# Kernel optimization log

Measured on AMD Instinct MI355X. Metric: run time of the kernel, lower is better.

## Reference

```python
import jax, jax.numpy as jnp
import numpy as np

B, S, V, D, E, F, H, HS, TOPK = 8, 512, 32000, 1024, 8, 4096, 8, 128, 2
NEG = -1e9


def _ln(x, g, b):
    m = x.mean(-1, keepdims=True)
    v = jnp.var(x, axis=-1, keepdims=True)
    return (x - m) * jax.lax.rsqrt(v + 1e-5) * g + b


def _attn(x, Wq, Wk, Wv, Wo, bo):
    q = (x @ Wq).reshape(B, S, H, HS)
    k = (x @ Wk).reshape(B, S, H, HS)
    v = (x @ Wv).reshape(B, S, H, HS)
    att = jnp.einsum('bqhd,bkhd->bhqk', q, k) * (HS ** -0.5)
    causal = jnp.tril(jnp.ones((S, S), bool))
    att = jax.nn.softmax(jnp.where(causal, att, NEG), axis=-1)
    o = jnp.einsum('bhqk,bkhd->bqhd', att, v).reshape(B, S, H * HS)
    return o @ Wo + bo


def _moe(x, noise, Wr, br, Wn, bn, W1, b1, W2, b2):
    # NoisyTopkRouter: logits + randn * softplus(noise_logits), top-k, -inf fill, softmax
    logits = x @ Wr + br                                   # [B,S,E]
    noisy = logits + noise * jax.nn.softplus(x @ Wn + bn)
    _, idx = jax.lax.top_k(noisy, TOPK)                    # [B,S,K]
    mask = jax.nn.one_hot(idx, E, dtype=jnp.bool_).any(-2)  # [B,S,E]
    gate = jax.nn.softmax(jnp.where(mask, noisy, NEG), axis=-1)
    # dense all-expert FFN; combine with gate (gate==0 for non-selected experts,
    # so this equals the original sparse per-expert dispatch/scatter math)
    xf = x.reshape(-1, D)                                   # [T,D]
    gf = gate.reshape(-1, E)                                # [T,E]
    h = jax.nn.relu(jnp.einsum('td,edf->etf', xf, W1) + b1[:, None, :])
    y = jnp.einsum('etf,efd->etd', h, W2) + b2[:, None, :]
    out = jnp.einsum('etd,te->td', y, gf).reshape(x.shape)
    return out, gate


def setup_inputs() -> dict:
    key = jax.random.key(0)
    ks = jax.random.split(key, 24)
    n = lambda i, shp, sc=0.02: jax.random.normal(ks[i], shp, jnp.float32) * sc
    return dict(
        input_ids=jax.random.randint(ks[0], (B, S), 0, V),
        attention_mask=jnp.ones((B, S), jnp.int32),
        emb=n(1, (V, D), 1.0),
        pos=n(2, (1, S, D), 1.0),
        Wq=n(3, (D, H * HS)), Wk=n(4, (D, H * HS)), Wv=n(5, (D, H * HS)),
        Wo=n(6, (H * HS, D)), bo=jnp.zeros((D,)),
        g1=jnp.ones((D,)), be1=jnp.zeros((D,)),
        g2=jnp.ones((D,)), be2=jnp.zeros((D,)),
        g3=jnp.ones((D,)), be3=jnp.zeros((D,)),
        Wr1=n(7, (D, E)), br1=jnp.zeros((E,)), Wn1=n(8, (D, E)), bn1=jnp.zeros((E,)),
        W1a=n(9, (E, D, F)), b1a=jnp.zeros((E, F)), W2a=n(10, (E, F, D)), b2a=jnp.zeros((E, D)),
        Wr2=n(11, (D, E)), br2=jnp.zeros((E,)), Wn2=n(12, (D, E)), bn2=jnp.zeros((E,)),
        W1b=n(13, (E, D, F)), b1b=jnp.zeros((E, F)), W2b=n(14, (E, F, D)), b2b=jnp.zeros((E, D)),
        noise1=jax.random.normal(ks[15], (B, S, E), jnp.float32),
        noise2=jax.random.normal(ks[16], (B, S, E), jnp.float32),
        Wc=n(17, (D, 10)), bc=jnp.zeros((10,)),
    )


def reference(input_ids, attention_mask, emb, pos, Wq, Wk, Wv, Wo, bo,
              g1, be1, g2, be2, g3, be3,
              Wr1, br1, Wn1, bn1, W1a, b1a, W2a, b2a,
              Wr2, br2, Wn2, bn2, W1b, b1b, W2b, b2b,
              noise1, noise2, Wc, bc):
    x = emb[input_ids]                                     # [B,S,D]
    x = x + _attn(_ln(x, g1, be1), Wq, Wk, Wv, Wo, bo)
    x = x + pos                                            # dropout = identity (eval)
    first, _ = _moe(_ln(x, g2, be2), noise1, Wr1, br1, Wn1, bn1, W1a, b1a, W2a, b2a)
    second, _ = _moe(_ln(x, g3, be3), noise2, Wr2, br2, Wn2, bn2, W1b, b1b, W2b, b2b)
    feature = second.mean(axis=1)                          # [B,D]
    cls = feature @ Wc + bc                                # [B,10]
    return (first, second, feature, cls)
```

## Files before the change

kernel.cpp:

```cpp
#include <hip/hip_runtime.h>
#include <cstdint>

typedef unsigned short u16;
typedef __attribute__((ext_vector_type(8))) __bf16 bf16x8;
typedef __attribute__((ext_vector_type(4))) float f32x4;

#define TOK 4096
#define DM  1024
#define EXP 8
#define FF  4096
#define SEQ 512
#define NH  8
#define HD  128
#define JOBCAP 18432

__device__ __forceinline__ u16 f2bf(float f) {
  union { float f; unsigned int u; } v; v.f = f;
  unsigned int u = v.u;
  u += 0x7FFFu + ((u >> 16) & 1u);
  return (u16)(u >> 16);
}
__device__ __forceinline__ float bf2f(u16 h) {
  union { unsigned int u; float f; } v; v.u = ((unsigned int)h) << 16; return v.f;
}

__device__ __forceinline__ void gl_lds16(const u16* g, u16* l) {
  __builtin_amdgcn_global_load_lds(
      (const __attribute__((address_space(1))) unsigned int*)g,
      (__attribute__((address_space(3))) unsigned int*)l, 16, 0, 0);
}

__global__ void k_embed(const int* __restrict__ ids, const float* __restrict__ emb,
                        float* __restrict__ x) {
  int t = blockIdx.x;
  int id = ids[t];
  const float4* src = (const float4*)(emb + (size_t)id * DM);
  float4* dst = (float4*)(x + (size_t)t * DM);
  dst[threadIdx.x] = src[threadIdx.x];
}

__global__ void k_lnrouter(const float* __restrict__ xin, const float* __restrict__ g,
                           const float* __restrict__ be,
                           const float* __restrict__ Wr, const float* __restrict__ br,
                           const float* __restrict__ Wn, const float* __restrict__ bn,
                           const float* __restrict__ noise,
                           u16* __restrict__ obf,
                           float* __restrict__ gates, int* __restrict__ topidx) {
  int t = blockIdx.x, tid = threadIdx.x;
  float4 v = ((const float4*)(xin + (size_t)t * DM))[tid];
  float s = v.x + v.y + v.z + v.w;
  float sq = v.x*v.x + v.y*v.y + v.z*v.z + v.w*v.w;
  for (int o = 32; o; o >>= 1) { s += __shfl_down(s, o); sq += __shfl_down(sq, o); }
  __shared__ float ss[4], sqs[4];
  if ((tid & 63) == 0) { ss[tid >> 6] = s; sqs[tid >> 6] = sq; }
  __syncthreads();
  s  = ss[0] + ss[1] + ss[2] + ss[3];
  sq = sqs[0] + sqs[1] + sqs[2] + sqs[3];
  float mean = s * (1.f / DM);
  float var  = sq * (1.f / DM) - mean * mean;
  float rstd = rsqrtf(var + 1e-5f);
  float4 gg = ((const float4*)g)[tid];
  float4 bb = ((const float4*)be)[tid];
  float xl[4];
  xl[0] = (v.x - mean) * rstd * gg.x + bb.x;
  xl[1] = (v.y - mean) * rstd * gg.y + bb.y;
  xl[2] = (v.z - mean) * rstd * gg.z + bb.z;
  xl[3] = (v.w - mean) * rstd * gg.w + bb.w;
  ushort4 u;
  u.x = f2bf(xl[0]); u.y = f2bf(xl[1]); u.z = f2bf(xl[2]); u.w = f2bf(xl[3]);
  ((ushort4*)(obf + (size_t)t * DM))[tid] = u;

  float pl[8], pn[8];
  #pragma unroll
  for (int e = 0; e < 8; e++) { pl[e] = 0.f; pn[e] = 0.f; }
  #pragma unroll
  for (int j = 0; j < 4; j++) {
    int d = tid * 4 + j;
    float xv = xl[j];
    const float4* wr = (const float4*)(Wr + (size_t)d * 8);
    const float4* wn = (const float4*)(Wn + (size_t)d * 8);
    float4 a0 = wr[0], a1 = wr[1], c0 = wn[0], c1 = wn[1];
    pl[0] += xv * a0.x; pl[1] += xv * a0.y; pl[2] += xv * a0.z; pl[3] += xv * a0.w;
    pl[4] += xv * a1.x; pl[5] += xv * a1.y; pl[6] += xv * a1.z; pl[7] += xv * a1.w;
    pn[0] += xv * c0.x; pn[1] += xv * c0.y; pn[2] += xv * c0.z; pn[3] += xv * c0.w;
    pn[4] += xv * c1.x; pn[5] += xv * c1.y; pn[6] += xv * c1.z; pn[7] += xv * c1.w;
  }
  for (int o = 32; o; o >>= 1) {
    #pragma unroll
    for (int e = 0; e < 8; e++) { pl[e] += __shfl_down(pl[e], o); pn[e] += __shfl_down(pn[e], o); }
  }
  __shared__ float sl[4][8], sn[4][8];
  if ((tid & 63) == 0) {
    int w = tid >> 6;
    #pragma unroll
    for (int e = 0; e < 8; e++) { sl[w][e] = pl[e]; sn[w][e] = pn[e]; }
  }
  __syncthreads();
  if (tid == 0) {
    float noisy[8];
    #pragma unroll
    for (int e = 0; e < 8; e++) {
      float l  = sl[0][e] + sl[1][e] + sl[2][e] + sl[3][e] + br[e];
      float nn = sn[0][e] + sn[1][e] + sn[2][e] + sn[3][e] + bn[e];
      float sp = (nn > 20.f) ? nn : log1pf(expf(nn));
      noisy[e] = l + noise[(size_t)t * 8 + e] * sp;
    }
    int i0 = 0;
    for (int e = 1; e < 8; e++) if (noisy[e] > noisy[i0]) i0 = e;
    int i1 = (i0 == 0) ? 1 : 0;
    for (int e = 0; e < 8; e++) if (e != i0 && noisy[e] > noisy[i1]) i1 = e;
    float e1 = expf(noisy[i1] - noisy[i0]);
    float zz = 1.f + e1;
    gates[t * 2] = 1.f / zz; gates[t * 2 + 1] = e1 / zz;
    topidx[t * 2] = i0; topidx[t * 2 + 1] = i1;
  }
}

__global__ void k_ln2(const float* __restrict__ in, const float* __restrict__ g,
                      const float* __restrict__ be, u16* __restrict__ oh,
                      u16* __restrict__ ol) {
  int t = blockIdx.x, tid = threadIdx.x;
  float4 v = ((const float4*)(in + (size_t)t * DM))[tid];
  float s = v.x + v.y + v.z + v.w;
  float sq = v.x*v.x + v.y*v.y + v.z*v.z + v.w*v.w;
  for (int o = 32; o; o >>= 1) { s += __shfl_down(s, o); sq += __shfl_down(sq, o); }
  __shared__ float ss[4], sqs[4];
  if ((tid & 63) == 0) { ss[tid >> 6] = s; sqs[tid >> 6] = sq; }
  __syncthreads();
  s  = ss[0] + ss[1] + ss[2] + ss[3];
  sq = sqs[0] + sqs[1] + sqs[2] + sqs[3];
  float mean = s * (1.f / DM);
  float var  = sq * (1.f / DM) - mean * mean;
  float rstd = rsqrtf(var + 1e-5f);
  float4 gg = ((const float4*)g)[tid];
  float4 bb = ((const float4*)be)[tid];
  float o4[4];
  o4[0] = (v.x - mean) * rstd * gg.x + bb.x;
  o4[1] = (v.y - mean) * rstd * gg.y + bb.y;
  o4[2] = (v.z - mean) * rstd * gg.z + bb.z;
  o4[3] = (v.w - mean) * rstd * gg.w + bb.w;
  ushort4 uh, ul;
  u16* ph = (u16*)&uh; u16* pl = (u16*)&ul;
  #pragma unroll
  for (int i = 0; i < 4; i++) {
    u16 hi = f2bf(o4[i]); ph[i] = hi; pl[i] = f2bf(o4[i] - bf2f(hi));
  }
  ((ushort4*)(oh + (size_t)t * DM))[tid] = uh;
  ((ushort4*)(ol + (size_t)t * DM))[tid] = ul;
}

__global__ void k_tcvt_split4(const float* __restrict__ Wq, const float* __restrict__ Wk,
                              const float* __restrict__ Wv, const float* __restrict__ Wo,
                              u16* __restrict__ qkvh, u16* __restrict__ qkvl,
                              u16* __restrict__ oh, u16* __restrict__ ol) {
  __shared__ float t[32][33];
  int z = blockIdx.z;
  const float* src = (z == 0) ? Wq : (z == 1) ? Wk : (z == 2) ? Wv : Wo;
  u16* dh = (z < 3) ? qkvh + (size_t)z * DM * DM : oh;
  u16* dl = (z < 3) ? qkvl + (size_t)z * DM * DM : ol;
  int k0 = blockIdx.x * 32, n0 = blockIdx.y * 32;
  int tx = threadIdx.x, ty = threadIdx.y;
  #pragma unroll
  for (int i = 0; i < 4; i++) t[ty + 8*i][tx] = src[(size_t)(k0 + ty + 8*i) * DM + n0 + tx];
  __syncthreads();
  int u = ty * 32 + tx;
  int r = u >> 3, kq = u & 7;
  ushort4 ohv, olv;
  u16* ph = (u16*)&ohv; u16* pl = (u16*)&olv;
  #pragma unroll
  for (int i = 0; i < 4; i++) {
    float v = t[kq*4+i][r];
    u16 hi = f2bf(v); ph[i] = hi; pl[i] = f2bf(v - bf2f(hi));
  }
  *(ushort4*)&dh[(size_t)(n0 + r) * DM + k0 + kq*4] = ohv;
  *(ushort4*)&dl[(size_t)(n0 + r) * DM + k0 + kq*4] = olv;
}

__global__ void k_tcvt64(const float* __restrict__ srcA, const float* __restrict__ srcB,
                         u16* __restrict__ dst, int K, int N) {
  __shared__ float t[64][65];
  int z = blockIdx.z;
  const float* src = (z < 8) ? srcA + (size_t)z * K * N : srcB + (size_t)(z - 8) * K * N;
  u16* d = dst + (size_t)z * K * N;
  int k0 = blockIdx.x * 64, n0 = blockIdx.y * 64;
  int u = threadIdx.y * 32 + threadIdx.x;
  #pragma unroll
  for (int i = 0; i < 4; i++) {
    int idx = u + i * 256;
    int kr = idx >> 4, nq = (idx & 15) * 4;
    float4 v = *(const float4*)&src[(size_t)(k0 + kr) * N + n0 + nq];
    t[kr][nq] = v.x; t[kr][nq+1] = v.y; t[kr][nq+2] = v.z; t[kr][nq+3] = v.w;
  }
  __syncthreads();
  #pragma unroll
  for (int j = 0; j < 2; j++) {
    int idx = u + j * 256;
    int nr = idx >> 3, kq = (idx & 7) * 8;
    ushort4 o0, o1;
    u16* p0 = (u16*)&o0; u16* p1 = (u16*)&o1;
    #pragma unroll
    for (int i = 0; i < 4; i++) p0[i] = f2bf(t[kq + i][nr]);
    #pragma unroll
    for (int i = 0; i < 4; i++) p1[i] = f2bf(t[kq + 4 + i][nr]);
    *(ushort4*)&d[(size_t)(n0 + nr) * K + k0 + kq]     = o0;
    *(ushort4*)&d[(size_t)(n0 + nr) * K + k0 + kq + 4] = o1;
  }
}

__global__ void k_softmax_h(float* __restrict__ scores) {
  int q = blockIdx.x, bh = blockIdx.y, tid = threadIdx.x;
  float* row = scores + ((size_t)bh * 512 + q) * 512;
  u16* orow = (u16*)row;
  const float scale = 0.088388347648318447f;
  int j0 = tid * 2;
  float v0 = -1e30f, v1 = -1e30f;
  if (j0 <= q)     v0 = row[j0] * scale;
  if (j0 + 1 <= q) v1 = row[j0 + 1] * scale;
  float m = fmaxf(v0, v1);
  for (int o = 32; o; o >>= 1) m = fmaxf(m, __shfl_down(m, o));
  __shared__ float sm[4], ssum[4];
  if ((tid & 63) == 0) sm[tid >> 6] = m;
  __syncthreads();
  m = fmaxf(fmaxf(sm[0], sm[1]), fmaxf(sm[2], sm[3]));
  float p0 = (j0 <= q)     ? expf(v0 - m) : 0.f;
  float p1 = (j0 + 1 <= q) ? expf(v1 - m) : 0.f;
  float s = p0 + p1;
  for (int o = 32; o; o >>= 1) s += __shfl_down(s, o);
  if ((tid & 63) == 0) ssum[tid >> 6] = s;
  __syncthreads();
  s = ssum[0] + ssum[1] + ssum[2] + ssum[3];
  float inv = 1.f / s;
  float pi0 = p0 * inv, pi1 = p1 * inv;
  u16 h0 = f2bf(pi0), h1 = f2bf(pi1);
  orow[j0]       = h0; orow[j0 + 1]       = h1;
  orow[512 + j0] = f2bf(pi0 - bf2f(h0));
  orow[512 + j0 + 1] = f2bf(pi1 - bf2f(h1));
}

constexpr int HOP_QKV    = 0;
constexpr int HOP_SCORES = 1;
constexpr int HOP_PV     = 2;
constexpr int HOP_PROJ   = 3;

struct GemmHArgs {
  const u16 *Ah, *Al, *Bh, *Bl;
  u16 *D0h, *D0l, *D1h, *D1l, *D2h, *D2l;
  float *Cf;
  const float *bias, *resid, *pos;
  int lda, ldb, K;
};

template<int OP>
__launch_bounds__(256, 4)
__global__ void gemm_h(GemmHArgs p) {
  int bx, by, z;
  if constexpr (OP == HOP_QKV) {
    int bid = blockIdx.x; int xcd = bid & 7, slot = bid >> 3;
    by = xcd * 3 + (slot >> 5); bx = slot & 31; z = 0;
  } else if constexpr (OP == HOP_PROJ) {
    int bid = blockIdx.x; by = bid & 7; bx = bid >> 3; z = 0;
  } else if constexpr (OP == HOP_SCORES) {
    int bid = blockIdx.x; z = bid / 10; int t = bid % 10;
    bx = (t >= 6) ? 3 : (t >= 3) ? 2 : (t >= 1) ? 1 : 0;
    by = t - ((bx * (bx + 1)) >> 1);
  } else {
    bx = blockIdx.x; by = blockIdx.y; z = blockIdx.z;
  }

  const u16 *Ahb, *Alb, *Bhb, *Blb;
  if constexpr (OP == HOP_SCORES) {
    size_t off = (size_t)(z >> 3) * 524288 + (size_t)(z & 7) * 128;
    Ahb = p.Ah + off; Alb = p.Al + off; Bhb = p.Bh + off; Blb = p.Bl + off;
  } else if constexpr (OP == HOP_PV) {
    size_t aoff = (size_t)z * 524288;
    Ahb = p.Ah + aoff; Alb = p.Ah + aoff + 512;
    size_t boff = (size_t)z * 65536;
    Bhb = p.Bh + boff; Blb = p.Bl + boff;
  } else {
    Ahb = p.Ah; Alb = p.Al; Bhb = p.Bh; Blb = p.Bl;
  }

  int kmax = p.K;
  if constexpr (OP == HOP_PV) { int lim = bx * 128 + 128; kmax = lim < p.K ? lim : p.K; }
  int nt = kmax >> 5;

  __shared__ __align__(16) u16 As[2 * 4096];
  __shared__ __align__(16) u16 Bs[2 * 4096];

  int tid = threadIdx.x, lane = tid & 63, wid = tid >> 6;
  int srow = wid * 16 + (lane >> 2), skoff = (lane & 3) * 8;
  int lo0 = (wid * 16) * 32, lo1 = ((wid + 4) * 16) * 32;
  int wr = wid >> 1, wc = wid & 1, fm = lane & 15, fk = (lane >> 4) * 8;

  f32x4 acc[4][4] = {};
  const size_t lda = p.lda, ldb = p.ldb;

  #pragma unroll 1
  for (int pass = 0; pass < 3; ++pass) {
    const u16* Ab = (pass < 2) ? Ahb : Alb;
    const u16* Bb = (pass & 1) ? Blb : Bhb;
    const u16* aptr0 = Ab + (size_t)(bx * 128 + srow) * lda + skoff;
    const u16* aptr1 = Ab + (size_t)(bx * 128 + 64 + srow) * lda + skoff;
    const u16* bptr0 = Bb + (size_t)(by * 128 + srow) * ldb + skoff;
    const u16* bptr1 = Bb + (size_t)(by * 128 + 64 + srow) * ldb + skoff;

    gl_lds16(aptr0, &As[lo0]); gl_lds16(aptr1, &As[lo1]);
    gl_lds16(bptr0, &Bs[lo0]); gl_lds16(bptr1, &Bs[lo1]);
    __syncthreads();
    int cur = 0;
    for (int t = 0; t < nt; ++t) {
      if (t + 1 < nt) {
        int nxt = (cur ^ 1) * 4096;
        int k0 = (t + 1) * 32;
        gl_lds16(aptr0 + k0, &As[nxt + lo0]); gl_lds16(aptr1 + k0, &As[nxt + lo1]);
        gl_lds16(bptr0 + k0, &Bs[nxt + lo0]); gl_lds16(bptr1 + k0, &Bs[nxt + lo1]);
      }
      int cb = cur * 4096;
      bf16x8 af[4], bfr[4];
      #pragma unroll
      for (int i = 0; i < 4; ++i) {
        af[i]  = *(const bf16x8*)&As[cb + (wr * 64 + i * 16 + fm) * 32 + fk];
        bfr[i] = *(const bf16x8*)&Bs[cb + (wc * 64 + i * 16 + fm) * 32 + fk];
      }
      #pragma unroll
      for (int mi = 0; mi < 4; ++mi)
        #pragma unroll
        for (int ni = 0; ni < 4; ++ni)
          acc[mi][ni] = __builtin_amdgcn_mfma_f32_16x16x32_bf16(af[mi], bfr[ni], acc[mi][ni], 0, 0, 0);
      __syncthreads();
      cur ^= 1;
    }
  }

  int rb = (lane >> 4) * 4, cl = lane & 15;
  #pragma unroll
  for (int mi = 0; mi < 4; ++mi)
    #pragma unroll
    for (int ni = 0; ni < 4; ++ni)
      #pragma unroll
      for (int j = 0; j < 4; ++j) {
        int m = bx * 128 + wr * 64 + mi * 16 + rb + j;
        int n = by * 128 + wc * 64 + ni * 16 + cl;
        float v = acc[mi][ni][j];
        if constexpr (OP == HOP_QKV) {
          u16 hi = f2bf(v); u16 lo = f2bf(v - bf2f(hi));
          int sel = n >> 10, nn = n & 1023;
          if (sel == 0) {
            p.D0h[(size_t)m * DM + nn] = hi; p.D0l[(size_t)m * DM + nn] = lo;
          } else if (sel == 1) {
            p.D1h[(size_t)m * DM + nn] = hi; p.D1l[(size_t)m * DM + nn] = lo;
          } else {
            size_t idx = (size_t)((m >> 9) * 8 + (nn >> 7)) * 65536 + (size_t)(nn & 127) * 512 + (m & 511);
            p.D2h[idx] = hi; p.D2l[idx] = lo;
          }
        } else if constexpr (OP == HOP_SCORES) {
          p.Cf[(size_t)z * 262144 + (size_t)m * 512 + n] = v;
        } else if constexpr (OP == HOP_PV) {
          u16 hi = f2bf(v); u16 lo = f2bf(v - bf2f(hi));
          size_t idx = (size_t)(z >> 3) * 524288 + (size_t)m * 1024 + (size_t)(z & 7) * 128 + n;
          p.D0h[idx] = hi; p.D0l[idx] = lo;
        } else {
          size_t idx = (size_t)m * 1024 + n;
          p.Cf[idx] = v + p.bias[n] + p.resid[idx] + p.pos[(size_t)(m & 511) * 1024 + n];
        }
      }
}

constexpr int OP_MOE1 = 0;
constexpr int OP_MOE2 = 1;

struct GemmArgs {
  const u16* A; const u16* B; void* C;
  const float* b1a; const float* b1b;
  const int* joblist; const int* seg;
  int lda, ldb, K;
};

template<int OP>
__launch_bounds__(256)
__global__ void gemm_k(GemmArgs p) {
  int bid = blockIdx.x;
  int xcd = bid & 7, slot = bid >> 3;
  int bx, by;
  if constexpr (OP == OP_MOE1) {
    by = xcd * 4 + (slot & 3);
    bx = slot >> 2;
  } else {
    bx = xcd * 18 + (slot >> 3);
    by = slot & 7;
  }
  int r0g = bx * 128;
  if (r0g >= p.seg[16]) return;
  int z = 0;
  #pragma unroll
  for (int e = 1; e < 16; ++e) z += (r0g >= p.seg[e]) ? 1 : 0;
  const u16* Bbase = p.B + (size_t)z * 4194304;
  const float* bias = (z < 8) ? p.b1a + (size_t)z * (OP == OP_MOE1 ? FF : DM)
                              : p.b1b + (size_t)(z - 8) * (OP == OP_MOE1 ? FF : DM);

  __shared__ __align__(16) u16 As[2 * 4096];
  __shared__ __align__(16) u16 Bs[2 * 4096];

  int tid = threadIdx.x;
  int lane = tid & 63, wid = tid >> 6;

  int srow = wid * 16 + (lane >> 2);
  int skoff = (lane & 3) * 8;

  const u16 *aptr0, *aptr1;
  if constexpr (OP == OP_MOE1) {
    int j0 = p.joblist[r0g + srow];
    int j1 = p.joblist[r0g + 64 + srow];
    aptr0 = p.A + (size_t)(j0 < 0 ? 0 : j0) * p.lda + skoff;
    aptr1 = p.A + (size_t)(j1 < 0 ? 0 : j1) * p.lda + skoff;
  } else {
    aptr0 = p.A + (size_t)(r0g + srow) * p.lda + skoff;
    aptr1 = p.A + (size_t)(r0g + 64 + srow) * p.lda + skoff;
  }
  const u16* bptr0 = Bbase + (size_t)(by * 128 + srow) * p.ldb + skoff;
  const u16* bptr1 = Bbase + (size_t)(by * 128 + 64 + srow) * p.ldb + skoff;

  int lo0 = (wid * 16) * 32;
  int lo1 = ((wid + 4) * 16) * 32;

  int wr = wid >> 1, wc = wid & 1;
  int fm = lane & 15;
  int fk = (lane >> 4) * 8;

  f32x4 acc[4][4] = {};
  int nt = p.K >> 5;

  gl_lds16(aptr0, &As[lo0]); gl_lds16(aptr1, &As[lo1]);
  gl_lds16(bptr0, &Bs[lo0]); gl_lds16(bptr1, &Bs[lo1]);
  __syncthreads();

  int cur = 0;
  for (int t = 0; t < nt; ++t) {
    if (t + 1 < nt) {
      int nxt = (cur ^ 1) * 4096;
      int k0 = (t + 1) * 32;
      gl_lds16(aptr0 + k0, &As[nxt + lo0]); gl_lds16(aptr1 + k0, &As[nxt + lo1]);
      gl_lds16(bptr0 + k0, &Bs[nxt + lo0]); gl_lds16(bptr1 + k0, &Bs[nxt + lo1]);
    }
    int cb = cur * 4096;
    bf16x8 af[4], bfr[4];
    #pragma unroll
    for (int i = 0; i < 4; ++i) {
      af[i]  = *(const bf16x8*)&As[cb + (wr * 64 + i * 16 + fm) * 32 + fk];
      bfr[i] = *(const bf16x8*)&Bs[cb + (wc * 64 + i * 16 + fm) * 32 + fk];
    }
    #pragma unroll
    for (int mi = 0; mi < 4; ++mi)
      #pragma unroll
      for (int ni = 0; ni < 4; ++ni)
        acc[mi][ni] = __builtin_amdgcn_mfma_f32_16x16x32_bf16(af[mi], bfr[ni], acc[mi][ni], 0, 0, 0);
    __syncthreads();
    cur ^= 1;
  }

  int rb = (lane >> 4) * 4;
  int cl = lane & 15;
  #pragma unroll
  for (int mi = 0; mi < 4; ++mi)
    #pragma unroll
    for (int ni = 0; ni < 4; ++ni)
      #pragma unroll
      for (int j = 0; j < 4; ++j) {
        int m = r0g + wr * 64 + mi * 16 + rb + j;
        int n = by * 128 + wc * 64 + ni * 16 + cl;
        float v = acc[mi][ni][j] + bias[n];
        if constexpr (OP == OP_MOE1) {
          v = v > 0.f ? v : 0.f;
          ((u16*)p.C)[(size_t)m * FF + n] = f2bf(v);
        } else {
          ((u16*)p.C)[(size_t)m * DM + n] = f2bf(v);
        }
      }
}

__global__ void k_moe_init(int* cnt, int* cnt2, int* joblist) {
  int i = blockIdx.x * 256 + threadIdx.x;
  if (i < JOBCAP) joblist[i] = -1;
  if (i < 16) { cnt[i] = 0; cnt2[i] = 0; }
}
__global__ void k_moe_count(const int* __restrict__ topidx, int* __restrict__ cnt) {
  int t = blockIdx.x * 256 + threadIdx.x;
  if (t >= 2 * TOK) return;
  int lo = (t >= TOK) ? 8 : 0;
  atomicAdd(&cnt[topidx[t * 2] + lo], 1);
  atomicAdd(&cnt[topidx[t * 2 + 1] + lo], 1);
}
__global__ void k_moe_offsets(const int* __restrict__ cnt, int* __restrict__ seg) {
  if (threadIdx.x == 0) {
    int o = 0;
    for (int e = 0; e < 16; e++) { seg[e] = o; o += (cnt[e] + 127) & ~127; }
    seg[16] = o;
  }
}
__global__ void k_moe_scatter(const int* __restrict__ topidx, int* __restrict__ cnt2,
                              const int* __restrict__ seg, int* __restrict__ joblist,
                              int* __restrict__ tokpos) {
  int t = blockIdx.x * 256 + threadIdx.x;
  if (t >= 2 * TOK) return;
  int lo = (t >= TOK) ? 8 : 0;
  #pragma unroll
  for (int s = 0; s < 2; s++) {
    int e = topidx[t * 2 + s] + lo;
    int p = atomicAdd(&cnt2[e], 1);
    int pos = seg[e] + p;
    joblist[pos] = t;
    tokpos[t * 2 + s] = pos;
  }
}
__global__ void k_combine(const u16* __restrict__ y, const float* __restrict__ gates,
                          const int* __restrict__ tokpos, float* __restrict__ out) {
  int t = blockIdx.x, tid = threadIdx.x;
  int p0 = tokpos[t * 2], p1 = tokpos[t * 2 + 1];
  float g0 = gates[t * 2], g1 = gates[t * 2 + 1];
  ushort4 a = ((const ushort4*)(y + (size_t)p0 * DM))[tid];
  ushort4 b = ((const ushort4*)(y + (size_t)p1 * DM))[tid];
  float4 o;
  o.x = g0 * bf2f(a.x) + g1 * bf2f(b.x);
  o.y = g0 * bf2f(a.y) + g1 * bf2f(b.y);
  o.z = g0 * bf2f(a.z) + g1 * bf2f(b.z);
  o.w = g0 * bf2f(a.w) + g1 * bf2f(b.w);
  ((float4*)(out + (size_t)t * DM))[tid] = o;
}

__global__ void k_feat1(const float* __restrict__ second, float* __restrict__ part) {
  int b = blockIdx.x, c = blockIdx.y, tid = threadIdx.x;
  const float* p = second + ((size_t)b * SEQ + (size_t)c * 64) * DM;
  float4 s = {0.f, 0.f, 0.f, 0.f};
  for (int j = 0; j < 64; ++j) {
    float4 v = ((const float4*)(p + (size_t)j * DM))[tid];
    s.x += v.x; s.y += v.y; s.z += v.z; s.w += v.w;
  }
  ((float4*)(part + (size_t)(b * 8 + c) * DM))[tid] = s;
}
__global__ void k_feat2(const float* __restrict__ part, float* __restrict__ feat) {
  int i = blockIdx.x * 256 + threadIdx.x;
  int b = i >> 10, d = i & 1023;
  float s = 0.f;
  #pragma unroll
  for (int c = 0; c < 8; ++c) s += part[(size_t)(b * 8 + c) * DM + d];
  feat[i] = s * (1.f / SEQ);
}
__global__ void k_cls(const float* __restrict__ feat, const float* __restrict__ Wc,
                      const float* __restrict__ bc, float* __restrict__ cls) {
  int o = blockIdx.x; int b = o / 10, n = o % 10; int l = threadIdx.x;
  float s = 0.f;
  for (int d = l; d < DM; d += 64) s += feat[b * DM + d] * Wc[(size_t)d * 10 + n];
  for (int off = 32; off; off >>= 1) s += __shfl_down(s, off);
  if (l == 0) cls[o] = s + bc[n];
}

extern "C" void kernel_launch(void* const* d_in, const int* in_sizes, int n_in,
                              void* d_out, int out_size, void* d_ws, size_t ws_size,
                              hipStream_t stream) {
  const int*   ids    = (const int*)d_in[0];
  const float* emb    = (const float*)d_in[2];
  const float* pos    = (const float*)d_in[3];
  const float* Wq     = (const float*)d_in[4];
  const float* Wk     = (const float*)d_in[5];
  const float* Wv     = (const float*)d_in[6];
  const float* Wo     = (const float*)d_in[7];
  const float* bo     = (const float*)d_in[8];
  const float* g1     = (const float*)d_in[9];
  const float* be1    = (const float*)d_in[10];
  const float* g2     = (const float*)d_in[11];
  const float* be2    = (const float*)d_in[12];
  const float* g3     = (const float*)d_in[13];
  const float* be3    = (const float*)d_in[14];
  const float* Wr1    = (const float*)d_in[15];
  const float* br1    = (const float*)d_in[16];
  const float* Wn1    = (const float*)d_in[17];
  const float* bn1    = (const float*)d_in[18];
  const float* W1a    = (const float*)d_in[19];
  const float* b1a    = (const float*)d_in[20];
  const float* W2a    = (const float*)d_in[21];
  const float* b2a    = (const float*)d_in[22];
  const float* Wr2    = (const float*)d_in[23];
  const float* br2    = (const float*)d_in[24];
  const float* Wn2    = (const float*)d_in[25];
  const float* bn2    = (const float*)d_in[26];
  const float* W1b    = (const float*)d_in[27];
  const float* b1b    = (const float*)d_in[28];
  const float* W2b    = (const float*)d_in[29];
  const float* b2b    = (const float*)d_in[30];
  const float* noise1 = (const float*)d_in[31];
  const float* noise2 = (const float*)d_in[32];
  const float* Wc     = (const float*)d_in[33];
  const float* bc     = (const float*)d_in[34];

  char* wsp = (char*)d_ws; size_t off = 0;
  auto alloc = [&](size_t bytes) -> void* {
    void* p = wsp + off; off += (bytes + 255) & ~(size_t)255; return p;
  };
  char*  G     = (char*)alloc(360710144);
  float* x     = (float*)alloc((size_t)TOK * DM * 4);
  float* x2    = (float*)alloc((size_t)TOK * DM * 4);
  u16*   xlnb  = (u16*)alloc((size_t)2 * TOK * DM * 2);
  float* gates  = (float*)alloc(2 * TOK * 2 * 4);
  int*   topidx = (int*)alloc(2 * TOK * 2 * 4);
  int*   cnt    = (int*)alloc(16 * 4);
  int*   cnt2   = (int*)alloc(16 * 4);
  int*   seg    = (int*)alloc(24 * 4);
  int*   joblist= (int*)alloc(JOBCAP * 4);
  int*   tokpos = (int*)alloc(2 * TOK * 2 * 4);
  float* fpart  = (float*)alloc(64 * DM * 4);
  (void)ws_size; (void)in_sizes; (void)n_in; (void)out_size;

  u16* WQKVTh = (u16*)(G + 0);
  u16* WQKVTl = (u16*)(G + 6291456);
  u16* WOTh   = (u16*)(G + 12582912);
  u16* WOTl   = (u16*)(G + 14680064);
  u16* XLNH   = (u16*)(G + 16777216);
  u16* XLNL   = (u16*)(G + 25165824);
  u16* QH     = (u16*)(G + 33554432);
  u16* QL     = (u16*)(G + 41943040);
  u16* KH     = (u16*)(G + 50331648);
  u16* KL     = (u16*)(G + 58720256);
  u16* VTh    = (u16*)(G + 67108864);
  u16* VTl    = (u16*)(G + 75497472);
  u16* OH     = (u16*)(G + 83886080);
  u16* OL     = (u16*)(G + 92274688);
  float* SC   = (float*)(G + 100663296);
  u16*   H    = (u16*)(G + 0);
  u16*   Y    = (u16*)(G + 150994944);
  u16*   WBUF = (u16*)(G + 226492416);

  float* out_first  = (float*)d_out;
  float* out_second = out_first + (size_t)TOK * DM;
  float* feat       = out_first + (size_t)2 * TOK * DM;
  float* cls        = feat + 8 * DM;

  dim3 tb(32, 8);
  hipLaunchKernelGGL(k_tcvt_split4, dim3(32, 32, 4), tb, 0, stream, Wq, Wk, Wv, Wo,
                     WQKVTh, WQKVTl, WOTh, WOTl);
  hipLaunchKernelGGL(k_embed, dim3(TOK), dim3(256), 0, stream, ids, emb, x);
  hipLaunchKernelGGL(k_ln2, dim3(TOK), dim3(256), 0, stream, x, g1, be1, XLNH, XLNL);

  GemmHArgs qa{};
  qa.Ah = XLNH; qa.Al = XLNL; qa.Bh = WQKVTh; qa.Bl = WQKVTl;
  qa.D0h = QH; qa.D0l = QL; qa.D1h = KH; qa.D1l = KL; qa.D2h = VTh; qa.D2l = VTl;
  qa.lda = DM; qa.ldb = DM; qa.K = DM;
  hipLaunchKernelGGL(gemm_h<HOP_QKV>, dim3(768), dim3(256), 0, stream, qa);

  GemmHArgs sa{};
  sa.Ah = QH; sa.Al = QL; sa.Bh = KH; sa.Bl = KL; sa.Cf = SC;
  sa.lda = DM; sa.ldb = DM; sa.K = HD;
  hipLaunchKernelGGL(gemm_h<HOP_SCORES>, dim3(640), dim3(256), 0, stream, sa);
  hipLaunchKernelGGL(k_softmax_h, dim3(SEQ, 64), dim3(256), 0, stream, SC);

  GemmHArgs pa{};
  pa.Ah = (const u16*)SC; pa.Bh = VTh; pa.Bl = VTl;
  pa.D0h = OH; pa.D0l = OL;
  pa.lda = 1024; pa.ldb = 512; pa.K = SEQ;
  hipLaunchKernelGGL(gemm_h<HOP_PV>, dim3(4, 1, 64), dim3(256), 0, stream, pa);

  GemmHArgs pj{};
  pj.Ah = OH; pj.Al = OL; pj.Bh = WOTh; pj.Bl = WOTl; pj.Cf = x2;
  pj.bias = bo; pj.resid = x; pj.pos = pos;
  pj.lda = DM; pj.ldb = DM; pj.K = DM;
  hipLaunchKernelGGL(gemm_h<HOP_PROJ>, dim3(256), dim3(256), 0, stream, pj);

  hipLaunchKernelGGL(k_lnrouter, dim3(TOK), dim3(256), 0, stream, x2, g2, be2,
                     Wr1, br1, Wn1, bn1, noise1, xlnb, gates, topidx);
  hipLaunchKernelGGL(k_lnrouter, dim3(TOK), dim3(256), 0, stream, x2, g3, be3,
                     Wr2, br2, Wn2, bn2, noise2, xlnb + (size_t)TOK * DM,
                     gates + (size_t)TOK * 2, topidx + (size_t)TOK * 2);
  hipLaunchKernelGGL(k_moe_init, dim3(72), dim3(256), 0, stream, cnt, cnt2, joblist);
  hipLaunchKernelGGL(k_moe_count, dim3(32), dim3(256), 0, stream, topidx, cnt);
  hipLaunchKernelGGL(k_moe_offsets, dim3(1), dim3(64), 0, stream, cnt, seg);
  hipLaunchKernelGGL(k_moe_scatter, dim3(32), dim3(256), 0, stream, topidx, cnt2, seg, joblist, tokpos);

  hipLaunchKernelGGL(k_tcvt64, dim3(16, 64, 16), tb, 0, stream, W1a, W1b, WBUF, DM, FF);
  GemmArgs m1{};
  m1.A = xlnb; m1.B = WBUF; m1.C = H; m1.b1a = b1a; m1.b1b = b1b;
  m1.joblist = joblist; m1.seg = seg;
  m1.lda = DM; m1.ldb = DM; m1.K = DM;
  hipLaunchKernelGGL(gemm_k<OP_MOE1>, dim3(4608), dim3(256), 0, stream, m1);

  hipLaunchKernelGGL(k_tcvt64, dim3(64, 16, 16), tb, 0, stream, W2a, W2b, WBUF, FF, DM);
  GemmArgs m2{};
  m2.A = H; m2.B = WBUF; m2.C = Y; m2.b1a = b2a; m2.b1b = b2b;
  m2.joblist = joblist; m2.seg = seg;
  m2.lda = FF; m2.ldb = FF; m2.K = FF;
  hipLaunchKernelGGL(gemm_k<OP_MOE2>, dim3(1152), dim3(256), 0, stream, m2);

  hipLaunchKernelGGL(k_combine, dim3(TOK), dim3(256), 0, stream, Y, gates, tokpos, out_first);
  hipLaunchKernelGGL(k_combine, dim3(TOK), dim3(256), 0, stream, Y,
                     gates + (size_t)TOK * 2, tokpos + (size_t)TOK * 2, out_second);

  hipLaunchKernelGGL(k_feat1, dim3(8, 8), dim3(256), 0, stream, out_second, fpart);
  hipLaunchKernelGGL(k_feat2, dim3(32), dim3(256), 0, stream, fpart, feat);
  hipLaunchKernelGGL(k_cls, dim3(80), dim3(64), 0, stream, feat, Wc, bc, cls);
}
```

Measured before the change: 1.125 ms.

## Fuse three split-bf16 GEMM passes into one K loop with shared tiles

The attention GEMM computed the hi*hi, hi*lo and lo*hi products of split-bf16 operands in three separate passes over K, reloading the A and B tiles each pass. The loop is restructured to stage the hi and lo tiles of A and B together and issue all three MFMA groups per K step. Each hi tile is now loaded once instead of twice and the number of loop iterations and barriers drops. The cost is doubled LDS use (64KB) and more live fragment registers, and the occupancy hint of 4 blocks per CU in the launch bounds is removed, which may reduce occupancy.

```diff
diff --git a/kernel.cpp b/kernel.cpp
--- a/kernel.cpp
+++ b/kernel.cpp
@@ -251,7 +251,7 @@
 };
 
 template<int OP>
-__launch_bounds__(256, 4)
+__launch_bounds__(256)
 __global__ void gemm_h(GemmHArgs p) {
   int bx, by, z;
   if constexpr (OP == HOP_QKV) {
@@ -284,53 +284,65 @@
   if constexpr (OP == HOP_PV) { int lim = bx * 128 + 128; kmax = lim < p.K ? lim : p.K; }
   int nt = kmax >> 5;
 
-  __shared__ __align__(16) u16 As[2 * 4096];
-  __shared__ __align__(16) u16 Bs[2 * 4096];
+  __shared__ __align__(16) u16 Ahs[2 * 4096];
+  __shared__ __align__(16) u16 Als[2 * 4096];
+  __shared__ __align__(16) u16 Bhs[2 * 4096];
+  __shared__ __align__(16) u16 Bls[2 * 4096];
 
   int tid = threadIdx.x, lane = tid & 63, wid = tid >> 6;
   int srow = wid * 16 + (lane >> 2), skoff = (lane & 3) * 8;
   int lo0 = (wid * 16) * 32, lo1 = ((wid + 4) * 16) * 32;
   int wr = wid >> 1, wc = wid & 1, fm = lane & 15, fk = (lane >> 4) * 8;
 
+  const size_t lda = p.lda, ldb = p.ldb;
+  size_t ar0 = (size_t)(bx * 128 + srow) * lda + skoff;
+  size_t ar1 = (size_t)(bx * 128 + 64 + srow) * lda + skoff;
+  size_t br0 = (size_t)(by * 128 + srow) * ldb + skoff;
+  size_t br1 = (size_t)(by * 128 + 64 + srow) * ldb + skoff;
+
   f32x4 acc[4][4] = {};
-  const size_t lda = p.lda, ldb = p.ldb;
-
-  #pragma unroll 1
-  for (int pass = 0; pass < 3; ++pass) {
-    const u16* Ab = (pass < 2) ? Ahb : Alb;
-    const u16* Bb = (pass & 1) ? Blb : Bhb;
-    const u16* aptr0 = Ab + (size_t)(bx * 128 + srow) * lda + skoff;
-    const u16* aptr1 = Ab + (size_t)(bx * 128 + 64 + srow) * lda + skoff;
-    const u16* bptr0 = Bb + (size_t)(by * 128 + srow) * ldb + skoff;
-    const u16* bptr1 = Bb + (size_t)(by * 128 + 64 + srow) * ldb + skoff;
-
-    gl_lds16(aptr0, &As[lo0]); gl_lds16(aptr1, &As[lo1]);
-    gl_lds16(bptr0, &Bs[lo0]); gl_lds16(bptr1, &Bs[lo1]);
+
+#define STAGE_H(BUF, K0) { int _b = (BUF) * 4096;                          \
+    gl_lds16(Ahb + ar0 + (K0), &Ahs[_b + lo0]); gl_lds16(Ahb + ar1 + (K0), &Ahs[_b + lo1]); \
+    gl_lds16(Alb + ar0 + (K0), &Als[_b + lo0]); gl_lds16(Alb + ar1 + (K0), &Als[_b + lo1]); \
+    gl_lds16(Bhb + br0 + (K0), &Bhs[_b + lo0]); gl_lds16(Bhb + br1 + (K0), &Bhs[_b + lo1]); \
+    gl_lds16(Blb + br0 + (K0), &Bls[_b + lo0]); gl_lds16(Blb + br1 + (K0), &Bls[_b + lo1]); }
+
+  STAGE_H(0, 0);
+  __syncthreads();
+  int cur = 0;
+  for (int t = 0; t < nt; ++t) {
+    if (t + 1 < nt) STAGE_H(cur ^ 1, (t + 1) * 32);
+    int cb = cur * 4096;
+    bf16x8 ah[4], al_[4], bh[4], bl[4];
+    #pragma unroll
+    for (int i = 0; i < 4; ++i) {
+      int ao = cb + (wr * 64 + i * 16 + fm) * 32 + fk;
+      int bo = cb + (wc * 64 + i * 16 + fm) * 32 + fk;
+      ah[i]  = *(const bf16x8*)&Ahs[ao];
+      bh[i]  = *(const bf16x8*)&Bhs[bo];
+      al_[i] = *(const bf16x8*)&Als[ao];
+      bl[i]  = *(const bf16x8*)&Bls[bo];
+    }
+    #pragma unroll
+    for (int mi = 0; mi < 4; ++mi)
+      #pragma unroll
+      for (int ni = 0; ni < 4; ++ni)
+        acc[mi][ni] = __builtin_amdgcn_mfma_f32_16x16x32_bf16(ah[mi], bh[ni], acc[mi][ni], 0, 0, 0);
+    #pragma unroll
+    for (int mi = 0; mi < 4; ++mi)
+      #pragma unroll
+      for (int ni = 0; ni < 4; ++ni)
+        acc[mi][ni] = __builtin_amdgcn_mfma_f32_16x16x32_bf16(ah[mi], bl[ni], acc[mi][ni], 0, 0, 0);
+    #pragma unroll
+    for (int mi = 0; mi < 4; ++mi)
+      #pragma unroll
+      for (int ni = 0; ni < 4; ++ni)
+        acc[mi][ni] = __builtin_amdgcn_mfma_f32_16x16x32_bf16(al_[mi], bh[ni], acc[mi][ni], 0, 0, 0);
     __syncthreads();
-    int cur = 0;
-    for (int t = 0; t < nt; ++t) {
-      if (t + 1 < nt) {
-        int nxt = (cur ^ 1) * 4096;
-        int k0 = (t + 1) * 32;
-        gl_lds16(aptr0 + k0, &As[nxt + lo0]); gl_lds16(aptr1 + k0, &As[nxt + lo1]);
-        gl_lds16(bptr0 + k0, &Bs[nxt + lo0]); gl_lds16(bptr1 + k0, &Bs[nxt + lo1]);
-      }
-      int cb = cur * 4096;
-      bf16x8 af[4], bfr[4];
-      #pragma unroll
-      for (int i = 0; i < 4; ++i) {
-        af[i]  = *(const bf16x8*)&As[cb + (wr * 64 + i * 16 + fm) * 32 + fk];
-        bfr[i] = *(const bf16x8*)&Bs[cb + (wc * 64 + i * 16 + fm) * 32 + fk];
-      }
-      #pragma unroll
-      for (int mi = 0; mi < 4; ++mi)
-        #pragma unroll
-        for (int ni = 0; ni < 4; ++ni)
-          acc[mi][ni] = __builtin_amdgcn_mfma_f32_16x16x32_bf16(af[mi], bfr[ni], acc[mi][ni], 0, 0, 0);
-      __syncthreads();
-      cur ^= 1;
-    }
-  }
+    cur ^= 1;
+  }
+#undef STAGE_H
 
   int rb = (lane >> 4) * 4, cl = lane & 15;
   #pragma unroll
```

Result: no change. 1.116 ms (-0.8%).
